# Optimization experiments

Hardware: AMD Instinct MI355X
Metric: run time of the kernel (lower is better)

The kernel has to match this reference:

```python
import jax, jax.numpy as jnp
import numpy as np

IN_C, HID_C, OUT_C = 128, 256, 128
N_NODES, N_EDGES = 50000, 600000


def setup_inputs() -> dict:
    key = jax.random.key(0)
    ks = jax.random.split(key, 8)
    x = jax.random.normal(ks[0], (N_NODES, IN_C), dtype=jnp.float32)
    edge_index = jax.random.randint(ks[1], (2, N_EDGES), 0, N_NODES, dtype=jnp.int64)
    def glorot(k, shape):
        lim = np.sqrt(6.0 / (shape[0] + shape[1])).astype(np.float32)
        return jax.random.uniform(k, shape, dtype=jnp.float32, minval=-lim, maxval=lim)
    # PyG SAGEConv: out = lin_l(mean_aggr) + lin_r(x_root); bias only in lin_l
    W1_l = glorot(ks[2], (IN_C, HID_C)); b1 = jnp.zeros((HID_C,), jnp.float32)
    W1_r = glorot(ks[3], (IN_C, HID_C))
    W2_l = glorot(ks[4], (HID_C, OUT_C)); b2 = jnp.zeros((OUT_C,), jnp.float32)
    W2_r = glorot(ks[5], (HID_C, OUT_C))
    return {"x": x, "edge_index": edge_index, "W1_l": W1_l, "b1": b1, "W1_r": W1_r,
            "W2_l": W2_l, "b2": b2, "W2_r": W2_r}


def _sage_conv(x, src, dst, W_l, b, W_r):
    n = x.shape[0]
    msg = x[src]  # [E, C] gather from source nodes
    agg = jax.ops.segment_sum(msg, dst, num_segments=n)
    cnt = jax.ops.segment_sum(jnp.ones((src.shape[0],), x.dtype), dst, num_segments=n)
    agg = agg / jnp.maximum(cnt, 1.0)[:, None]  # mean aggregation, zero-deg safe
    return agg @ W_l + b + x @ W_r


def reference(x, edge_index, W1_l, b1, W1_r, W2_l, b2, W2_r):
    src, dst = edge_index[0], edge_index[1]
    h = jax.nn.relu(_sage_conv(x, src, dst, W1_l, b1, W1_r))
    return _sage_conv(h, src, dst, W2_l, b2, W2_r)
```

## Files before the change

kernel.cpp:

```cpp
#include <hip/hip_runtime.h>
#include <hip/hip_bf16.h>


#define N_NODES 50000
#define IN_C    128
#define HID_C   256
#define OUT_C   128
#define N_EDGES 600000
#define SLOTS   64

#define PB_FILL 586
#define PB_W1   (PB_FILL + 256)
#define PB_W2   (PB_W1 + 256)
#define PB_X    (PB_W2 + 6250)

typedef __attribute__((ext_vector_type(8))) short short8;
typedef __attribute__((ext_vector_type(4))) float f32x4;
typedef __attribute__((ext_vector_type(2))) float f32x2;

__device__ __forceinline__ float bf2f(short s) {
    union { unsigned u; float f; } c;
    c.u = ((unsigned)(unsigned short)s) << 16;
    return c.f;
}
__device__ __forceinline__ unsigned f2fp8(float v) {
    return (unsigned)__builtin_amdgcn_cvt_pk_fp8_f32(v, v, 0, false) & 0xffu;
}
__device__ __forceinline__ void acc_fp8x4(float* a, unsigned u) {
    f32x2 lo = __builtin_amdgcn_cvt_pk_f32_fp8(u, false);
    f32x2 hi = __builtin_amdgcn_cvt_pk_f32_fp8(u, true);
    a[0] += lo[0]; a[1] += lo[1]; a[2] += hi[0]; a[3] += hi[1];
}

__global__ __launch_bounds__(256) void prep(
    const float* __restrict__ x, __hip_bfloat16* __restrict__ xbf,
    const float* __restrict__ W1l, const float* __restrict__ W1r,
    const float* __restrict__ W2l, const float* __restrict__ W2r,
    __hip_bfloat16* __restrict__ W1t, __hip_bfloat16* __restrict__ W2t,
    const int* __restrict__ srcI, const int* __restrict__ dstI,
    int* __restrict__ cur, int* __restrict__ colp) {
    int b = blockIdx.x;
    if (b < PB_FILL) {
        int base = b * 1024 + threadIdx.x;
        #pragma unroll
        for (int k = 0; k < 4; ++k) {
            int e = base + k * 256;
            if (e < N_EDGES) {
                int d = dstI[e];
                int pos = atomicAdd(&cur[d], 1);
                if (pos < SLOTS) colp[(size_t)d * SLOTS + pos] = srcI[e];
            }
        }
    } else if (b < PB_W1) {
        int reg = b - PB_FILL;
        int half = reg >> 7;
        int t = (reg & 127) * 256 + threadIdx.x;
        int k = t >> 8, n = t & 255;
        const float* src = half ? W1r : W1l;
        W1t[n * 256 + half * 128 + k] = __float2bfloat16(src[t]);
    } else if (b < PB_W2) {
        int reg = b - PB_W1;
        int half = reg >> 7;
        int t = (reg & 127) * 256 + threadIdx.x;
        int k = t >> 7, n = t & 127;
        const float* src = half ? W2r : W2l;
        W2t[(size_t)(half * 128 + n) * 256 + k] = __float2bfloat16(src[t]);
    } else {
        int t = (b - PB_W2) * 256 + threadIdx.x;
        if (t >= N_NODES * 32) return;
        int row = t >> 5, c = (t & 31) * 4;
        float4 v = *(const float4*)(x + (size_t)row * 128 + c);
        __hip_bfloat16* d = xbf + (size_t)row * 128 + c;
        __hip_bfloat162 p0, p1;
        p0.x = __float2bfloat16(v.x); p0.y = __float2bfloat16(v.y);
        p1.x = __float2bfloat16(v.z); p1.y = __float2bfloat16(v.w);
        *(__hip_bfloat162*)d = p0;
        *(__hip_bfloat162*)(d + 2) = p1;
    }
}

__global__ __launch_bounds__(256, 4) void fused_fwd(
    const __hip_bfloat16* __restrict__ xbf,
    const int* __restrict__ deg, const int* __restrict__ colp,
    const __hip_bfloat16* __restrict__ W1t,
    const float* __restrict__ b1,
    const __hip_bfloat16* __restrict__ W2t,
    const float* __restrict__ b2,
    unsigned char* __restrict__ hp,
    float* __restrict__ pre,
    int M) {
    __shared__ __hip_bfloat16 hAB[64 * 256];

    int tid  = threadIdx.x;
    int wave = tid >> 6, lane = tid & 63;
    int mb   = blockIdx.x * 64;
    int sl   = tid & 15;

    for (int pass = 0; pass < 4; ++pass) {
        int r = pass * 16 + (tid >> 4);
        int node = mb + r; if (node >= M) node = M - 1;
        int d = deg[node]; if (d > SLOTS) d = SLOTS;
        const int* col = colp + (size_t)node * SLOTS;
        const __hip_bfloat16* base = xbf + sl * 8;
        float a[8];
        #pragma unroll
        for (int c = 0; c < 8; ++c) a[c] = 0.f;

        short8 v0, v1, v2, v3;
        int j = 0;
        if (d >= 4) {
            int s0 = col[0], s1 = col[1], s2 = col[2], s3 = col[3];
            v0 = *(const short8*)(base + (size_t)s0 * 128);
            v1 = *(const short8*)(base + (size_t)s1 * 128);
            v2 = *(const short8*)(base + (size_t)s2 * 128);
            v3 = *(const short8*)(base + (size_t)s3 * 128);
            for (; j + 8 <= d; j += 4) {
                int t0 = col[j + 4], t1 = col[j + 5];
                int t2 = col[j + 6], t3 = col[j + 7];
                short8 w0 = *(const short8*)(base + (size_t)t0 * 128);
                short8 w1 = *(const short8*)(base + (size_t)t1 * 128);
                short8 w2 = *(const short8*)(base + (size_t)t2 * 128);
                short8 w3 = *(const short8*)(base + (size_t)t3 * 128);
                #pragma unroll
                for (int c = 0; c < 8; ++c)
                    a[c] += (bf2f(v0[c]) + bf2f(v1[c])) + (bf2f(v2[c]) + bf2f(v3[c]));
                v0 = w0; v1 = w1; v2 = w2; v3 = w3;
            }
            #pragma unroll
            for (int c = 0; c < 8; ++c)
                a[c] += (bf2f(v0[c]) + bf2f(v1[c])) + (bf2f(v2[c]) + bf2f(v3[c]));
            j += 4;
        }
        int rem = d - j;
        if (rem > 0) {
            int s0 = col[j];
            int s1 = (rem > 1) ? col[j + 1] : s0;
            int s2 = (rem > 2) ? col[j + 2] : s0;
            short8 t0 = *(const short8*)(base + (size_t)s0 * 128);
            short8 t1 = *(const short8*)(base + (size_t)s1 * 128);
            short8 t2 = *(const short8*)(base + (size_t)s2 * 128);
            #pragma unroll
            for (int c = 0; c < 8; ++c) a[c] += bf2f(t0[c]);
            if (rem > 1) {
                #pragma unroll
                for (int c = 0; c < 8; ++c) a[c] += bf2f(t1[c]);
            }
            if (rem > 2) {
                #pragma unroll
                for (int c = 0; c < 8; ++c) a[c] += bf2f(t2[c]);
            }
        }

        float inv = 1.f / (float)max(d, 1);
        short8 q;
        #pragma unroll
        for (int c = 0; c < 8; ++c) {
            union { __hip_bfloat16 b; short s; } cv;
            cv.b = __float2bfloat16(a[c] * inv);
            q[c] = cv.s;
        }
        int pc = (sl & 8) | ((sl & 7) ^ (r & 7));
        *(short8*)&hAB[r * 256 + pc * 8] = q;
        short8 sv = *(const short8*)(xbf + (size_t)node * 128 + sl * 8);
        *(short8*)&hAB[r * 256 + (16 + pc) * 8] = sv;
    }
    __syncthreads();

    f32x4 acc[4][4];
    #pragma unroll
    for (int i = 0; i < 4; ++i)
        #pragma unroll
        for (int j = 0; j < 4; ++j)
            acc[i][j] = (f32x4){0.f, 0.f, 0.f, 0.f};

    for (int kt = 0; kt < 256; kt += 64) {
        #pragma unroll
        for (int ks = 0; ks < 64; ks += 32) {
            int chunkL = (ks >> 3) + (lane >> 4);
            short8 af[4], bf[4];
            #pragma unroll
            for (int j = 0; j < 4; ++j) {
                int brow = wave * 64 + j * 16 + (lane & 15);
                bf[j] = *(const short8*)(W1t + (size_t)brow * 256 + kt + ks
                                         + (lane >> 4) * 8);
            }
            #pragma unroll
            for (int i = 0; i < 4; ++i) {
                int row = i * 16 + (lane & 15);
                af[i] = *(const short8*)&hAB[row * 256 +
                        ((kt >> 3) + (chunkL ^ (row & 7))) * 8];
            }
            #pragma unroll
            for (int i = 0; i < 4; ++i)
                #pragma unroll
                for (int j = 0; j < 4; ++j)
                    acc[i][j] = __builtin_amdgcn_mfma_f32_16x16x32_bf16(
                        af[i], bf[j], acc[i][j], 0, 0, 0);
        }
    }
    __syncthreads();

    int cn[4];
    float bc[4];
    #pragma unroll
    for (int j = 0; j < 4; ++j) {
        cn[j] = wave * 64 + j * 16 + (lane & 15);
        bc[j] = b1[cn[j]];
    }
    #pragma unroll
    for (int i = 0; i < 4; ++i)
        #pragma unroll
        for (int r = 0; r < 4; ++r) {
            int row = i * 16 + (lane >> 4) * 4 + r;
            #pragma unroll
            for (int j = 0; j < 4; ++j) {
                float v = fmaxf(acc[i][j][r] + bc[j], 0.f);
                int c = cn[j] >> 3;
                int pchk = (c & ~7) | ((c & 7) ^ (row & 7));
                union { __hip_bfloat16 b; short s; } cv;
                cv.b = __float2bfloat16(v);
                *(short*)&hAB[row * 256 + pchk * 8 + (cn[j] & 7)] = cv.s;
            }
        }
    __syncthreads();

    #pragma unroll
    for (int i = 0; i < 4; ++i)
        #pragma unroll
        for (int j = 0; j < 4; ++j)
            acc[i][j] = (f32x4){0.f, 0.f, 0.f, 0.f};

    for (int kt = 0; kt < 256; kt += 64) {
        #pragma unroll
        for (int ks = 0; ks < 64; ks += 32) {
            int chunkL = (ks >> 3) + (lane >> 4);
            short8 af[4], bf[4];
            #pragma unroll
            for (int j = 0; j < 4; ++j) {
                int brow = wave * 64 + j * 16 + (lane & 15);
                bf[j] = *(const short8*)(W2t + (size_t)brow * 256 + kt + ks
                                         + (lane >> 4) * 8);
            }
            #pragma unroll
            for (int i = 0; i < 4; ++i) {
                int row = i * 16 + (lane & 15);
                af[i] = *(const short8*)&hAB[row * 256 +
                        ((kt >> 3) + (chunkL ^ (row & 7))) * 8];
            }
            #pragma unroll
            for (int i = 0; i < 4; ++i)
                #pragma unroll
                for (int j = 0; j < 4; ++j)
                    acc[i][j] = __builtin_amdgcn_mfma_f32_16x16x32_bf16(
                        af[i], bf[j], acc[i][j], 0, 0, 0);
        }
    }

    if (wave < 2) {
        #pragma unroll
        for (int i = 0; i < 4; ++i)
            #pragma unroll
            for (int r = 0; r < 4; ++r) {
                int row = mb + i * 16 + (lane >> 4) * 4 + r;
                if (row >= M) continue;
                #pragma unroll
                for (int j = 0; j < 4; ++j)
                    hp[(size_t)row * 128 + cn[j]] = (unsigned char)f2fp8(acc[i][j][r]);
            }
    } else {
        float bc2[4];
        #pragma unroll
        for (int j = 0; j < 4; ++j) bc2[j] = b2[cn[j] - 128];
        #pragma unroll
        for (int i = 0; i < 4; ++i)
            #pragma unroll
            for (int r = 0; r < 4; ++r) {
                int row = mb + i * 16 + (lane >> 4) * 4 + r;
                if (row >= M) continue;
                #pragma unroll
                for (int j = 0; j < 4; ++j)
                    pre[(size_t)row * 128 + cn[j] - 128] = acc[i][j][r] + bc2[j];
            }
    }
}

__global__ __launch_bounds__(256) void aggregate_fp8_final(
    const unsigned char* __restrict__ feat,
    const int* __restrict__ deg, const int* __restrict__ colp,
    float* __restrict__ outp, const float* __restrict__ pre, int nNodes) {
    int node = blockIdx.x * 16 + (threadIdx.x >> 4);
    int sl   = threadIdx.x & 15;
    if (node >= nNodes) return;
    int beg = node * SLOTS;
    int d   = deg[node]; if (d > SLOTS) d = SLOTS;
    const int* col = colp;
    const unsigned char* base = feat + sl * 8;
    float a[8];
    #pragma unroll
    for (int c = 0; c < 8; ++c) a[c] = 0.f;

    uint2 v0, v1, v2, v3;
    int j = 0;
    if (d >= 4) {
        int s0 = col[beg + 0], s1 = col[beg + 1];
        int s2 = col[beg + 2], s3 = col[beg + 3];
        v0 = *(const uint2*)(base + (size_t)s0 * 128);
        v1 = *(const uint2*)(base + (size_t)s1 * 128);
        v2 = *(const uint2*)(base + (size_t)s2 * 128);
        v3 = *(const uint2*)(base + (size_t)s3 * 128);
        for (; j + 8 <= d; j += 4) {
            int t0 = col[beg + j + 4], t1 = col[beg + j + 5];
            int t2 = col[beg + j + 6], t3 = col[beg + j + 7];
            uint2 w0 = *(const uint2*)(base + (size_t)t0 * 128);
            uint2 w1 = *(const uint2*)(base + (size_t)t1 * 128);
            uint2 w2 = *(const uint2*)(base + (size_t)t2 * 128);
            uint2 w3 = *(const uint2*)(base + (size_t)t3 * 128);
            acc_fp8x4(a,     v0.x); acc_fp8x4(a,     v1.x);
            acc_fp8x4(a,     v2.x); acc_fp8x4(a,     v3.x);
            acc_fp8x4(a + 4, v0.y); acc_fp8x4(a + 4, v1.y);
            acc_fp8x4(a + 4, v2.y); acc_fp8x4(a + 4, v3.y);
            v0 = w0; v1 = w1; v2 = w2; v3 = w3;
        }
        acc_fp8x4(a,     v0.x); acc_fp8x4(a,     v1.x);
        acc_fp8x4(a,     v2.x); acc_fp8x4(a,     v3.x);
        acc_fp8x4(a + 4, v0.y); acc_fp8x4(a + 4, v1.y);
        acc_fp8x4(a + 4, v2.y); acc_fp8x4(a + 4, v3.y);
        j += 4;
    }
    for (; j < d; ++j) {
        uint2 v = *(const uint2*)(base + (size_t)col[beg + j] * 128);
        acc_fp8x4(a, v.x);
        acc_fp8x4(a + 4, v.y);
    }

    float inv = 1.f / (float)max(d, 1);
    const float* pp = pre + (size_t)node * 128 + sl * 8;
    float* op = outp + (size_t)node * 128 + sl * 8;
    float4 p0 = *(const float4*)pp;
    float4 p1 = *(const float4*)(pp + 4);
    *(float4*)op       = make_float4(a[0] * inv + p0.x, a[1] * inv + p0.y,
                                     a[2] * inv + p0.z, a[3] * inv + p0.w);
    *(float4*)(op + 4) = make_float4(a[4] * inv + p1.x, a[5] * inv + p1.y,
                                     a[6] * inv + p1.z, a[7] * inv + p1.w);
}

extern "C" void kernel_launch(void* const* d_in, const int* in_sizes, int n_in,
                              void* d_out, int out_size, void* d_ws, size_t ws_size,
                              hipStream_t stream) {
    const float* x    = (const float*)d_in[0];
    const int*   ei   = (const int*)d_in[1];
    const float* W1l  = (const float*)d_in[2];
    const float* b1   = (const float*)d_in[3];
    const float* W1r  = (const float*)d_in[4];
    const float* W2l  = (const float*)d_in[5];
    const float* b2   = (const float*)d_in[6];
    const float* W2r  = (const float*)d_in[7];
    float* out = (float*)d_out;

    const int N = N_NODES;
    const int* srcI = ei;
    const int* dstI = ei + N_EDGES;

    char* w = (char*)d_ws;
    int*            cur     = (int*)(w + 0);
    int*            colp    = (int*)(w + 204800);
    __hip_bfloat16* W1t     = (__hip_bfloat16*)(w + 13004800);
    __hip_bfloat16* W2t     = (__hip_bfloat16*)(w + 13135872);
    __hip_bfloat16* xbf     = (__hip_bfloat16*)(w + 13266944);
    unsigned char*  hp_f8   = (unsigned char*)(w + 26066944);
    float*          pre     = (float*)(w + 32466944);

    hipMemsetAsync(cur, 0, 200000, stream);
    prep<<<PB_X, 256, 0, stream>>>(x, xbf, W1l, W1r, W2l, W2r, W1t, W2t,
                                   srcI, dstI, cur, colp);

    fused_fwd<<<(N + 63) / 64, 256, 0, stream>>>(
        xbf, cur, colp, W1t, b1, W2t, b2, hp_f8, pre, N);

    aggregate_fp8_final<<<(N + 15) / 16, 256, 0, stream>>>(
        hp_f8, cur, colp, out, pre, N);
}
```

Baseline: 196.6 us.

## Store neighbor indices as 16-bit, vectorize index loads, deepen gather unroll

Neighbor indices in the padded adjacency table are now stored as unsigned 16-bit values, which fit because there are 50000 nodes. This halves the size of the table and lets each thread fetch 8 or 4 indices with a single vector load. Both gather loops now prefetch 8 neighbor rows per iteration instead of 4, for more memory-level parallelism. Nontemporal hints are added on the adjacency fill, the pre-activation output, and the final output. The cost is more registers per thread, and the 16-bit index format only works while the node count stays below 65536.

```diff
diff --git a/kernel.cpp b/kernel.cpp
--- a/kernel.cpp
+++ b/kernel.cpp
@@ -15,6 +15,8 @@
 #define PB_X    (PB_W2 + 6250)
 
 typedef __attribute__((ext_vector_type(8))) short short8;
+typedef __attribute__((ext_vector_type(8))) unsigned short ushort8;
+typedef __attribute__((ext_vector_type(4))) unsigned short ushort4u;
 typedef __attribute__((ext_vector_type(4))) float f32x4;
 typedef __attribute__((ext_vector_type(2))) float f32x2;
 
@@ -38,7 +40,7 @@
     const float* __restrict__ W2l, const float* __restrict__ W2r,
     __hip_bfloat16* __restrict__ W1t, __hip_bfloat16* __restrict__ W2t,
     const int* __restrict__ srcI, const int* __restrict__ dstI,
-    int* __restrict__ cur, int* __restrict__ colp) {
+    int* __restrict__ cur, unsigned short* __restrict__ colp) {
     int b = blockIdx.x;
     if (b < PB_FILL) {
         int base = b * 1024 + threadIdx.x;
@@ -48,7 +50,9 @@
             if (e < N_EDGES) {
                 int d = dstI[e];
                 int pos = atomicAdd(&cur[d], 1);
-                if (pos < SLOTS) colp[(size_t)d * SLOTS + pos] = srcI[e];
+                if (pos < SLOTS)
+                    __builtin_nontemporal_store(
+                        (unsigned short)srcI[e], &colp[(size_t)d * SLOTS + pos]);
             }
         }
     } else if (b < PB_W1) {
@@ -81,7 +85,7 @@
 
 __global__ __launch_bounds__(256, 4) void fused_fwd(
     const __hip_bfloat16* __restrict__ xbf,
-    const int* __restrict__ deg, const int* __restrict__ colp,
+    const int* __restrict__ deg, const unsigned short* __restrict__ colp,
     const __hip_bfloat16* __restrict__ W1t,
     const float* __restrict__ b1,
     const __hip_bfloat16* __restrict__ W2t,
@@ -100,32 +104,57 @@
         int r = pass * 16 + (tid >> 4);
         int node = mb + r; if (node >= M) node = M - 1;
         int d = deg[node]; if (d > SLOTS) d = SLOTS;
-        const int* col = colp + (size_t)node * SLOTS;
+        const unsigned short* col = colp + (size_t)node * SLOTS;
         const __hip_bfloat16* base = xbf + sl * 8;
         float a[8];
         #pragma unroll
         for (int c = 0; c < 8; ++c) a[c] = 0.f;
 
-        short8 v0, v1, v2, v3;
         int j = 0;
-        if (d >= 4) {
-            int s0 = col[0], s1 = col[1], s2 = col[2], s3 = col[3];
-            v0 = *(const short8*)(base + (size_t)s0 * 128);
-            v1 = *(const short8*)(base + (size_t)s1 * 128);
-            v2 = *(const short8*)(base + (size_t)s2 * 128);
-            v3 = *(const short8*)(base + (size_t)s3 * 128);
-            for (; j + 8 <= d; j += 4) {
-                int t0 = col[j + 4], t1 = col[j + 5];
-                int t2 = col[j + 6], t3 = col[j + 7];
-                short8 w0 = *(const short8*)(base + (size_t)t0 * 128);
-                short8 w1 = *(const short8*)(base + (size_t)t1 * 128);
-                short8 w2 = *(const short8*)(base + (size_t)t2 * 128);
-                short8 w3 = *(const short8*)(base + (size_t)t3 * 128);
+        if (d >= 8) {
+            ushort8 ci = __builtin_nontemporal_load((const ushort8*)col);
+            short8 v0 = *(const short8*)(base + (size_t)ci[0] * 128);
+            short8 v1 = *(const short8*)(base + (size_t)ci[1] * 128);
+            short8 v2 = *(const short8*)(base + (size_t)ci[2] * 128);
+            short8 v3 = *(const short8*)(base + (size_t)ci[3] * 128);
+            short8 v4 = *(const short8*)(base + (size_t)ci[4] * 128);
+            short8 v5 = *(const short8*)(base + (size_t)ci[5] * 128);
+            short8 v6 = *(const short8*)(base + (size_t)ci[6] * 128);
+            short8 v7 = *(const short8*)(base + (size_t)ci[7] * 128);
+            for (; j + 16 <= d; j += 8) {
+                ushort8 cx = __builtin_nontemporal_load(
+                                 (const ushort8*)(col + j + 8));
+                short8 w0 = *(const short8*)(base + (size_t)cx[0] * 128);
+                short8 w1 = *(const short8*)(base + (size_t)cx[1] * 128);
+                short8 w2 = *(const short8*)(base + (size_t)cx[2] * 128);
+                short8 w3 = *(const short8*)(base + (size_t)cx[3] * 128);
+                short8 w4 = *(const short8*)(base + (size_t)cx[4] * 128);
+                short8 w5 = *(const short8*)(base + (size_t)cx[5] * 128);
+                short8 w6 = *(const short8*)(base + (size_t)cx[6] * 128);
+                short8 w7 = *(const short8*)(base + (size_t)cx[7] * 128);
                 #pragma unroll
                 for (int c = 0; c < 8; ++c)
                     a[c] += (bf2f(v0[c]) + bf2f(v1[c])) + (bf2f(v2[c]) + bf2f(v3[c]));
+                #pragma unroll
+                for (int c = 0; c < 8; ++c)
+                    a[c] += (bf2f(v4[c]) + bf2f(v5[c])) + (bf2f(v6[c]) + bf2f(v7[c]));
                 v0 = w0; v1 = w1; v2 = w2; v3 = w3;
-            }
+                v4 = w4; v5 = w5; v6 = w6; v7 = w7;
+            }
+            #pragma unroll
+            for (int c = 0; c < 8; ++c)
+                a[c] += (bf2f(v0[c]) + bf2f(v1[c])) + (bf2f(v2[c]) + bf2f(v3[c]));
+            #pragma unroll
+            for (int c = 0; c < 8; ++c)
+                a[c] += (bf2f(v4[c]) + bf2f(v5[c])) + (bf2f(v6[c]) + bf2f(v7[c]));
+            j += 8;
+        }
+        if (d - j >= 4) {
+            ushort4u c4 = __builtin_nontemporal_load((const ushort4u*)(col + j));
+            short8 v0 = *(const short8*)(base + (size_t)c4[0] * 128);
+            short8 v1 = *(const short8*)(base + (size_t)c4[1] * 128);
+            short8 v2 = *(const short8*)(base + (size_t)c4[2] * 128);
+            short8 v3 = *(const short8*)(base + (size_t)c4[3] * 128);
             #pragma unroll
             for (int c = 0; c < 8; ++c)
                 a[c] += (bf2f(v0[c]) + bf2f(v1[c])) + (bf2f(v2[c]) + bf2f(v3[c]));
@@ -279,48 +308,75 @@
                 if (row >= M) continue;
                 #pragma unroll
                 for (int j = 0; j < 4; ++j)
-                    pre[(size_t)row * 128 + cn[j] - 128] = acc[i][j][r] + bc2[j];
+                    __builtin_nontemporal_store(
+                        acc[i][j][r] + bc2[j],
+                        &pre[(size_t)row * 128 + cn[j] - 128]);
             }
     }
 }
 
 __global__ __launch_bounds__(256) void aggregate_fp8_final(
     const unsigned char* __restrict__ feat,
-    const int* __restrict__ deg, const int* __restrict__ colp,
+    const int* __restrict__ deg, const unsigned short* __restrict__ colp,
     float* __restrict__ outp, const float* __restrict__ pre, int nNodes) {
     int node = blockIdx.x * 16 + (threadIdx.x >> 4);
     int sl   = threadIdx.x & 15;
     if (node >= nNodes) return;
-    int beg = node * SLOTS;
     int d   = deg[node]; if (d > SLOTS) d = SLOTS;
-    const int* col = colp;
+    const unsigned short* col = colp + (size_t)node * SLOTS;
     const unsigned char* base = feat + sl * 8;
     float a[8];
     #pragma unroll
     for (int c = 0; c < 8; ++c) a[c] = 0.f;
 
-    uint2 v0, v1, v2, v3;
     int j = 0;
-    if (d >= 4) {
-        int s0 = col[beg + 0], s1 = col[beg + 1];
-        int s2 = col[beg + 2], s3 = col[beg + 3];
-        v0 = *(const uint2*)(base + (size_t)s0 * 128);
-        v1 = *(const uint2*)(base + (size_t)s1 * 128);
-        v2 = *(const uint2*)(base + (size_t)s2 * 128);
-        v3 = *(const uint2*)(base + (size_t)s3 * 128);
-        for (; j + 8 <= d; j += 4) {
-            int t0 = col[beg + j + 4], t1 = col[beg + j + 5];
-            int t2 = col[beg + j + 6], t3 = col[beg + j + 7];
-            uint2 w0 = *(const uint2*)(base + (size_t)t0 * 128);
-            uint2 w1 = *(const uint2*)(base + (size_t)t1 * 128);
-            uint2 w2 = *(const uint2*)(base + (size_t)t2 * 128);
-            uint2 w3 = *(const uint2*)(base + (size_t)t3 * 128);
+    if (d >= 8) {
+        ushort8 ci = __builtin_nontemporal_load((const ushort8*)col);
+        uint2 v0 = *(const uint2*)(base + (size_t)ci[0] * 128);
+        uint2 v1 = *(const uint2*)(base + (size_t)ci[1] * 128);
+        uint2 v2 = *(const uint2*)(base + (size_t)ci[2] * 128);
+        uint2 v3 = *(const uint2*)(base + (size_t)ci[3] * 128);
+        uint2 v4 = *(const uint2*)(base + (size_t)ci[4] * 128);
+        uint2 v5 = *(const uint2*)(base + (size_t)ci[5] * 128);
+        uint2 v6 = *(const uint2*)(base + (size_t)ci[6] * 128);
+        uint2 v7 = *(const uint2*)(base + (size_t)ci[7] * 128);
+        for (; j + 16 <= d; j += 8) {
+            ushort8 cx = __builtin_nontemporal_load((const ushort8*)(col + j + 8));
+            uint2 w0 = *(const uint2*)(base + (size_t)cx[0] * 128);
+            uint2 w1 = *(const uint2*)(base + (size_t)cx[1] * 128);
+            uint2 w2 = *(const uint2*)(base + (size_t)cx[2] * 128);
+            uint2 w3 = *(const uint2*)(base + (size_t)cx[3] * 128);
+            uint2 w4 = *(const uint2*)(base + (size_t)cx[4] * 128);
+            uint2 w5 = *(const uint2*)(base + (size_t)cx[5] * 128);
+            uint2 w6 = *(const uint2*)(base + (size_t)cx[6] * 128);
+            uint2 w7 = *(const uint2*)(base + (size_t)cx[7] * 128);
             acc_fp8x4(a,     v0.x); acc_fp8x4(a,     v1.x);
             acc_fp8x4(a,     v2.x); acc_fp8x4(a,     v3.x);
             acc_fp8x4(a + 4, v0.y); acc_fp8x4(a + 4, v1.y);
             acc_fp8x4(a + 4, v2.y); acc_fp8x4(a + 4, v3.y);
+            acc_fp8x4(a,     v4.x); acc_fp8x4(a,     v5.x);
+            acc_fp8x4(a,     v6.x); acc_fp8x4(a,     v7.x);
+            acc_fp8x4(a + 4, v4.y); acc_fp8x4(a + 4, v5.y);
+            acc_fp8x4(a + 4, v6.y); acc_fp8x4(a + 4, v7.y);
             v0 = w0; v1 = w1; v2 = w2; v3 = w3;
-        }
+            v4 = w4; v5 = w5; v6 = w6; v7 = w7;
+        }
+        acc_fp8x4(a,     v0.x); acc_fp8x4(a,     v1.x);
+        acc_fp8x4(a,     v2.x); acc_fp8x4(a,     v3.x);
+        acc_fp8x4(a + 4, v0.y); acc_fp8x4(a + 4, v1.y);
+        acc_fp8x4(a + 4, v2.y); acc_fp8x4(a + 4, v3.y);
+        acc_fp8x4(a,     v4.x); acc_fp8x4(a,     v5.x);
+        acc_fp8x4(a,     v6.x); acc_fp8x4(a,     v7.x);
+        acc_fp8x4(a + 4, v4.y); acc_fp8x4(a + 4, v5.y);
+        acc_fp8x4(a + 4, v6.y); acc_fp8x4(a + 4, v7.y);
+        j += 8;
+    }
+    if (d - j >= 4) {
+        ushort4u c4 = __builtin_nontemporal_load((const ushort4u*)(col + j));
+        uint2 v0 = *(const uint2*)(base + (size_t)c4[0] * 128);
+        uint2 v1 = *(const uint2*)(base + (size_t)c4[1] * 128);
+        uint2 v2 = *(const uint2*)(base + (size_t)c4[2] * 128);
+        uint2 v3 = *(const uint2*)(base + (size_t)c4[3] * 128);
         acc_fp8x4(a,     v0.x); acc_fp8x4(a,     v1.x);
         acc_fp8x4(a,     v2.x); acc_fp8x4(a,     v3.x);
         acc_fp8x4(a + 4, v0.y); acc_fp8x4(a + 4, v1.y);
@@ -328,20 +384,22 @@
         j += 4;
     }
     for (; j < d; ++j) {
-        uint2 v = *(const uint2*)(base + (size_t)col[beg + j] * 128);
+        uint2 v = *(const uint2*)(base + (size_t)col[j] * 128);
         acc_fp8x4(a, v.x);
         acc_fp8x4(a + 4, v.y);
     }
 
     float inv = 1.f / (float)max(d, 1);
-    const float* pp = pre + (size_t)node * 128 + sl * 8;
-    float* op = outp + (size_t)node * 128 + sl * 8;
-    float4 p0 = *(const float4*)pp;
-    float4 p1 = *(const float4*)(pp + 4);
-    *(float4*)op       = make_float4(a[0] * inv + p0.x, a[1] * inv + p0.y,
-                                     a[2] * inv + p0.z, a[3] * inv + p0.w);
-    *(float4*)(op + 4) = make_float4(a[4] * inv + p1.x, a[5] * inv + p1.y,
-                                     a[6] * inv + p1.z, a[7] * inv + p1.w);
+    const f32x4* pp = (const f32x4*)(pre + (size_t)node * 128 + sl * 8);
+    f32x4 p0 = __builtin_nontemporal_load(pp);
+    f32x4 p1 = __builtin_nontemporal_load(pp + 1);
+    f32x4 o0 = {a[0] * inv + p0[0], a[1] * inv + p0[1],
+                a[2] * inv + p0[2], a[3] * inv + p0[3]};
+    f32x4 o1 = {a[4] * inv + p1[0], a[5] * inv + p1[1],
+                a[6] * inv + p1[2], a[7] * inv + p1[3]};
+    f32x4* op = (f32x4*)(outp + (size_t)node * 128 + sl * 8);
+    __builtin_nontemporal_store(o0, op);
+    __builtin_nontemporal_store(o1, op + 1);
 }
 
 extern "C" void kernel_launch(void* const* d_in, const int* in_sizes, int n_in,
@@ -362,13 +420,13 @@
     const int* dstI = ei + N_EDGES;
 
     char* w = (char*)d_ws;
-    int*            cur     = (int*)(w + 0);
-    int*            colp    = (int*)(w + 204800);
-    __hip_bfloat16* W1t     = (__hip_bfloat16*)(w + 13004800);
-    __hip_bfloat16* W2t     = (__hip_bfloat16*)(w + 13135872);
-    __hip_bfloat16* xbf     = (__hip_bfloat16*)(w + 13266944);
-    unsigned char*  hp_f8   = (unsigned char*)(w + 26066944);
-    float*          pre     = (float*)(w + 32466944);
+    int*             cur   = (int*)(w + 0);
+    unsigned short*  colp  = (unsigned short*)(w + 204800);
+    __hip_bfloat16*  W1t   = (__hip_bfloat16*)(w + 6604800);
+    __hip_bfloat16*  W2t   = (__hip_bfloat16*)(w + 6735872);
+    __hip_bfloat16*  xbf   = (__hip_bfloat16*)(w + 6866944);
+    unsigned char*   hp_f8 = (unsigned char*)(w + 19666944);
+    float*           pre   = (float*)(w + 26066944);
 
     hipMemsetAsync(cur, 0, 200000, stream);
     prep<<<PB_X, 256, 0, stream>>>(x, xbf, W1l, W1r, W2l, W2r, W1t, W2t,
```

Measured after the change: 201.0 us. 1.02x slower.
